# Kernel optimization log

Hardware: AMD Instinct MI355X
Metric: run time of the kernel (lower is better)

Reference implementation:

```python
import jax, jax.numpy as jnp
import numpy as np

POOL = 7      # AdaptiveMaxPool2d output size
CROP = 96     # max box side; all generated boxes fit inside a CROP x CROP window


def _adaptive_maxpool_box(feature_chw, coord):
    """PyTorch AdaptiveMaxPool2d((7,7)) on feature_chw[:, y1:y2, x1:x2].

    feature_chw: [2, H, W]; coord: int32 [4] = (y1, x1, y2, x2), with
    0 < y2-y1 <= CROP, 0 < x2-x1 <= CROP. Returns [2, 7, 7].
    """
    y1, x1, y2, x2 = coord[0], coord[1], coord[2], coord[3]
    crop = jax.lax.dynamic_slice(feature_chw, (0, y1, x1), (2, CROP, CROP))
    h = y2 - y1
    w = x2 - x1
    i = jnp.arange(POOL)
    r = jnp.arange(CROP)
    # PyTorch adaptive pooling bins: [floor(i*h/P), ceil((i+1)*h/P))
    sr = (i * h) // POOL
    er = ((i + 1) * h + POOL - 1) // POOL
    sc = (i * w) // POOL
    ec = ((i + 1) * w + POOL - 1) // POOL
    mask_r = (r[None, :] >= sr[:, None]) & (r[None, :] < er[:, None])  # [7, CROP]
    mask_c = (r[None, :] >= sc[:, None]) & (r[None, :] < ec[:, None])  # [7, CROP]
    neg = jnp.finfo(crop.dtype).min
    # row-wise max per output row: [7, 2, CROP]
    rowp = jnp.max(jnp.where(mask_r[:, None, :, None], crop[None], neg), axis=2)
    # col-wise max per output col: [7, 7, 2]
    out = jnp.max(jnp.where(mask_c[None, :, None, :], rowp[:, None], neg), axis=3)
    return jnp.transpose(out, (2, 0, 1))  # [2, 7, 7]


def setup_inputs() -> dict:
    key = jax.random.key(0)
    k1, k2, k3, k4, k5, k6 = jax.random.split(key, 6)
    N = 1024
    H = W = 2048
    feature = jax.random.normal(k1, (1, 2, H, W), jnp.float32)
    y1 = jax.random.randint(k2, (N,), 0, H - CROP)
    x1 = jax.random.randint(k3, (N,), 0, W - CROP)
    hh = jax.random.randint(k4, (N,), POOL, CROP)
    ww = jax.random.randint(k5, (N,), POOL, CROP)
    box_coords = jnp.stack([y1, x1, y1 + hh, x1 + ww], axis=1).astype(jnp.int32)
    boxes = jnp.concatenate(
        [jnp.zeros((N, 1), jnp.float32),
         jnp.arange(N, dtype=jnp.float32)[:, None],
         box_coords.astype(jnp.float32)], axis=1)  # [N, 6]
    fc_w = jax.random.normal(k6, (4, POOL * POOL * 2), jnp.float32) * 0.1
    fc_b = jnp.zeros((4,), jnp.float32)
    return {"feature": feature, "boxes": boxes, "box_coords": box_coords,
            "fc_w": fc_w, "fc_b": fc_b}


def reference(feature, boxes, box_coords, fc_w, fc_b):
    # per-box ROI adaptive max pool, batched with vmap: [N, 2, 7, 7]
    pooled = jax.vmap(lambda c: _adaptive_maxpool_box(feature[0], c))(box_coords)
    feat = pooled.reshape(pooled.shape[0], -1)        # [N, 98] (channel-major flatten)
    deltaB = jax.nn.relu(feat @ fc_w.T + fc_b)        # [N, 4]
    return boxes.at[:, 2:6].add(deltaB)               # boxes[:,2:6] += deltaB
```

## Files before the change

kernel.cpp:

```cpp
#include <hip/hip_runtime.h>
#include <float.h>

#define POOL 7
#define FW 2048
#define FH 2048
#define CROP 96
#define LROW 100

#define GLD16(gp, lp) __builtin_amdgcn_global_load_lds( \
    (const __attribute__((address_space(1))) void*)(gp), \
    (__attribute__((address_space(3))) void*)(lp), 16, 0, 0)

__global__ __launch_bounds__(256, 4) void roi_pool_fc_kernel(
    const float* __restrict__ feature,
    const float* __restrict__ boxes,
    const int*   __restrict__ coords,
    const float* __restrict__ fc_w,
    const float* __restrict__ fc_b,
    float* __restrict__ out,
    int N)
{
    const int n = blockIdx.x;
    const int t = threadIdx.x;

    __shared__ float lds[CROP * LROW];
    __shared__ float pooled[98];
    __shared__ float delta[4];

    const int4 cd = ((const int4*)coords)[n];
    const int y1 = cd.x;
    const int x1 = cd.y;
    const int h  = cd.z - y1;
    const int w  = cd.w - x1;

    const int x1a  = x1 & ~3;
    const int off  = x1 - x1a;
    const int wvec = (w + off + 3) >> 2;

    float wpre[4] = {0.f, 0.f, 0.f, 0.f};
    float bias = 0.f;
    if (t < 128) {
        const int oo = t >> 5, lane = t & 31;
        const float* wrow = fc_w + oo * 98;
        #pragma unroll
        for (int k = 0; k < 4; ++k) {
            const int idx = lane + 32 * k;
            if (idx < 98) wpre[k] = wrow[idx];
        }
        if (lane == 0) bias = fc_b[oo];
    }
    const float bx = (t < 6) ? boxes[n * 6 + t] : 0.f;

    const float* b0 = feature + (size_t)y1 * FW + x1a;
    const float* b1 = b0 + (size_t)FH * FW;
    const int wbase = t & 192;

    int   goff[10];
    bool  vok[10];
    #pragma unroll
    for (int k = 0; k < 10; ++k) {
        const int v = t + k * 256;
        const int r = v / 25;
        const int c4 = v - r * 25;
        goff[k] = r * FW + 4 * c4;
        vok[k]  = (v < 2400) && (r < h) && (c4 < wvec);
    }

    #pragma unroll
    for (int k = 0; k < 10; ++k) {
        char* lbase = (char*)lds + 16 * (wbase + k * 256);
        if (vok[k]) GLD16(b0 + goff[k], lbase);
    }
    float4 regs[10];
    #pragma unroll
    for (int k = 0; k < 10; ++k)
        regs[k] = vok[k] ? *(const float4*)(b1 + goff[k])
                         : make_float4(0.f, 0.f, 0.f, 0.f);

    const int o = t >> 2;
    const int s = t & 3;
    const int i = o / 7;
    const int j = o % 7;
    int sr = 0, er = 0, sc = 0, ec = 0, sc4 = 0, ec4 = 0;
    if (t < 196) {
        sr  = (i * h) / POOL;
        er  = ((i + 1) * h + POOL - 1) / POOL;
        sc  = (j * w) / POOL + off;
        ec  = ((j + 1) * w + POOL - 1) / POOL + off;
        sc4 = sc >> 2;
        ec4 = (ec + 3) >> 2;
    }

    __syncthreads();

    if (t < 196) {
        float m = -FLT_MAX;
        for (int r = sr + s; r < er; r += 4) {
            const float4* rowp = (const float4*)(lds + r * LROW);
            for (int c4 = sc4; c4 < ec4; ++c4) {
                const float4 v = rowp[c4];
                const int b = c4 * 4;
                m = fmaxf(m, (b + 0 >= sc && b + 0 < ec) ? v.x : -FLT_MAX);
                m = fmaxf(m, (b + 1 >= sc && b + 1 < ec) ? v.y : -FLT_MAX);
                m = fmaxf(m, (b + 2 >= sc && b + 2 < ec) ? v.z : -FLT_MAX);
                m = fmaxf(m, (b + 3 >= sc && b + 3 < ec) ? v.w : -FLT_MAX);
            }
        }
        m = fmaxf(m, __shfl_xor(m, 1, 64));
        m = fmaxf(m, __shfl_xor(m, 2, 64));
        if (s == 0) pooled[o] = m;
    }
    __syncthreads();

    #pragma unroll
    for (int k = 0; k < 10; ++k)
        if (vok[k]) *(float4*)((char*)lds + 16 * (t + k * 256)) = regs[k];
    __syncthreads();

    if (t < 196) {
        float m = -FLT_MAX;
        for (int r = sr + s; r < er; r += 4) {
            const float4* rowp = (const float4*)(lds + r * LROW);
            for (int c4 = sc4; c4 < ec4; ++c4) {
                const float4 v = rowp[c4];
                const int b = c4 * 4;
                m = fmaxf(m, (b + 0 >= sc && b + 0 < ec) ? v.x : -FLT_MAX);
                m = fmaxf(m, (b + 1 >= sc && b + 1 < ec) ? v.y : -FLT_MAX);
                m = fmaxf(m, (b + 2 >= sc && b + 2 < ec) ? v.z : -FLT_MAX);
                m = fmaxf(m, (b + 3 >= sc && b + 3 < ec) ? v.w : -FLT_MAX);
            }
        }
        m = fmaxf(m, __shfl_xor(m, 1, 64));
        m = fmaxf(m, __shfl_xor(m, 2, 64));
        if (s == 0) pooled[49 + o] = m;
    }
    __syncthreads();

    if (t < 128) {
        const int lane = t & 31;
        float acc = 0.f;
        #pragma unroll
        for (int k = 0; k < 4; ++k) {
            const int idx = lane + 32 * k;
            acc = fmaf(idx < 98 ? pooled[idx] : 0.f, wpre[k], acc);
        }
        #pragma unroll
        for (int mm = 16; mm; mm >>= 1)
            acc += __shfl_xor(acc, mm, 64);
        if (lane == 0) delta[t >> 5] = fmaxf(acc + bias, 0.f);
    }
    __syncthreads();

    if (t < 6)
        out[n * 6 + t] = bx + (t >= 2 ? delta[t - 2] : 0.f);
}

extern "C" void kernel_launch(void* const* d_in, const int* in_sizes, int n_in,
                              void* d_out, int out_size, void* d_ws, size_t ws_size,
                              hipStream_t stream) {
    const float* feature = (const float*)d_in[0];
    const float* boxes   = (const float*)d_in[1];
    const int*   coords  = (const int*)d_in[2];
    const float* fc_w    = (const float*)d_in[3];
    const float* fc_b    = (const float*)d_in[4];
    float* out = (float*)d_out;

    const int N = in_sizes[2] / 4;
    roi_pool_fc_kernel<<<N, 256, 0, stream>>>(feature, boxes, coords, fc_w, fc_b, out, N);
}
```

Baseline: 85.60 us.

## Load channel 1 via async global-to-LDS and mask bins with precomputed select

Channel 1 no longer goes through a register-staged prefetch. It is now loaded with a second round of direct global-to-LDS loads after channel 0 has been pooled. This frees 40 registers per thread, but the second load is serialized behind the first pool pass instead of overlapping with it. The bin-max inner loop now reads a fixed 5 float4s per row and masks each value with a precomputed fmin/fmax select array instead of per-element compares. LDS is padded by 8 floats so those fixed-width reads cannot run past the end.

```diff
diff --git a/kernel.cpp b/kernel.cpp
--- a/kernel.cpp
+++ b/kernel.cpp
@@ -23,7 +23,7 @@
     const int n = blockIdx.x;
     const int t = threadIdx.x;
 
-    __shared__ float lds[CROP * LROW];
+    __shared__ float lds[CROP * LROW + 8];
     __shared__ float pooled[98];
     __shared__ float delta[4];
 
@@ -55,8 +55,8 @@
     const float* b1 = b0 + (size_t)FH * FW;
     const int wbase = t & 192;
 
-    int   goff[10];
-    bool  vok[10];
+    int  goff[10];
+    bool vok[10];
     #pragma unroll
     for (int k = 0; k < 10; ++k) {
         const int v = t + k * 256;
@@ -71,68 +71,62 @@
         char* lbase = (char*)lds + 16 * (wbase + k * 256);
         if (vok[k]) GLD16(b0 + goff[k], lbase);
     }
-    float4 regs[10];
-    #pragma unroll
-    for (int k = 0; k < 10; ++k)
-        regs[k] = vok[k] ? *(const float4*)(b1 + goff[k])
-                         : make_float4(0.f, 0.f, 0.f, 0.f);
 
     const int o = t >> 2;
     const int s = t & 3;
     const int i = o / 7;
     const int j = o % 7;
-    int sr = 0, er = 0, sc = 0, ec = 0, sc4 = 0, ec4 = 0;
+    int sr = 0, er = 0, sc4 = 0;
+    float sel[20];
     if (t < 196) {
-        sr  = (i * h) / POOL;
-        er  = ((i + 1) * h + POOL - 1) / POOL;
-        sc  = (j * w) / POOL + off;
-        ec  = ((j + 1) * w + POOL - 1) / POOL + off;
+        sr = (i * h) / POOL;
+        er = ((i + 1) * h + POOL - 1) / POOL;
+        const int sc = (j * w) / POOL + off;
+        const int ec = ((j + 1) * w + POOL - 1) / POOL + off;
         sc4 = sc >> 2;
-        ec4 = (ec + 3) >> 2;
+        #pragma unroll
+        for (int q = 0; q < 20; ++q) {
+            const int b = sc4 * 4 + q;
+            sel[q] = (b >= sc && b < ec) ? FLT_MAX : -FLT_MAX;
+        }
     }
 
-    __syncthreads();
-
-    if (t < 196) {
+    auto binmax = [&]() -> float {
         float m = -FLT_MAX;
         for (int r = sr + s; r < er; r += 4) {
-            const float4* rowp = (const float4*)(lds + r * LROW);
-            for (int c4 = sc4; c4 < ec4; ++c4) {
-                const float4 v = rowp[c4];
-                const int b = c4 * 4;
-                m = fmaxf(m, (b + 0 >= sc && b + 0 < ec) ? v.x : -FLT_MAX);
-                m = fmaxf(m, (b + 1 >= sc && b + 1 < ec) ? v.y : -FLT_MAX);
-                m = fmaxf(m, (b + 2 >= sc && b + 2 < ec) ? v.z : -FLT_MAX);
-                m = fmaxf(m, (b + 3 >= sc && b + 3 < ec) ? v.w : -FLT_MAX);
+            const float4* rowp = (const float4*)(lds + r * LROW + 4 * sc4);
+            float4 v[5];
+            #pragma unroll
+            for (int q = 0; q < 5; ++q) v[q] = rowp[q];
+            #pragma unroll
+            for (int q = 0; q < 5; ++q) {
+                m = fmaxf(m, fminf(v[q].x, sel[4 * q + 0]));
+                m = fmaxf(m, fminf(v[q].y, sel[4 * q + 1]));
+                m = fmaxf(m, fminf(v[q].z, sel[4 * q + 2]));
+                m = fmaxf(m, fminf(v[q].w, sel[4 * q + 3]));
             }
         }
         m = fmaxf(m, __shfl_xor(m, 1, 64));
         m = fmaxf(m, __shfl_xor(m, 2, 64));
-        if (s == 0) pooled[o] = m;
+        return m;
+    };
+
+    __syncthreads();
+
+    float m0 = -FLT_MAX;
+    if (t < 196) m0 = binmax();
+    __syncthreads();
+
+    #pragma unroll
+    for (int k = 0; k < 10; ++k) {
+        char* lbase = (char*)lds + 16 * (wbase + k * 256);
+        if (vok[k]) GLD16(b1 + goff[k], lbase);
     }
     __syncthreads();
 
-    #pragma unroll
-    for (int k = 0; k < 10; ++k)
-        if (vok[k]) *(float4*)((char*)lds + 16 * (t + k * 256)) = regs[k];
-    __syncthreads();
-
     if (t < 196) {
-        float m = -FLT_MAX;
-        for (int r = sr + s; r < er; r += 4) {
-            const float4* rowp = (const float4*)(lds + r * LROW);
-            for (int c4 = sc4; c4 < ec4; ++c4) {
-                const float4 v = rowp[c4];
-                const int b = c4 * 4;
-                m = fmaxf(m, (b + 0 >= sc && b + 0 < ec) ? v.x : -FLT_MAX);
-                m = fmaxf(m, (b + 1 >= sc && b + 1 < ec) ? v.y : -FLT_MAX);
-                m = fmaxf(m, (b + 2 >= sc && b + 2 < ec) ? v.z : -FLT_MAX);
-                m = fmaxf(m, (b + 3 >= sc && b + 3 < ec) ? v.w : -FLT_MAX);
-            }
-        }
-        m = fmaxf(m, __shfl_xor(m, 1, 64));
-        m = fmaxf(m, __shfl_xor(m, 2, 64));
-        if (s == 0) pooled[49 + o] = m;
+        const float m1 = binmax();
+        if (s == 0) { pooled[o] = m0; pooled[49 + o] = m1; }
     }
     __syncthreads();
 
```

Measured after the change: 83.21 us. 1.03x faster.
